# Optimization experiments

Measured on AMD Instinct MI355X. Metric: run time of the kernel, lower is better.

The kernel has to match this reference:

```python
import jax, jax.numpy as jnp
import numpy as np

D_MODEL = 1024
NUM_HEADS = 16
HEAD_DIM = D_MODEL // NUM_HEADS


def setup_inputs() -> dict:
    key = jax.random.key(0)
    ks = jax.random.split(key, 9)
    s = 1.0 / np.sqrt(D_MODEL)
    return {
        "x": jax.random.normal(ks[0], (4, 2048, D_MODEL), dtype=jnp.float32),
        "Wq": jax.random.uniform(ks[1], (D_MODEL, D_MODEL), minval=-s, maxval=s, dtype=jnp.float32),
        "bq": jax.random.uniform(ks[2], (D_MODEL,), minval=-s, maxval=s, dtype=jnp.float32),
        "Wk": jax.random.uniform(ks[3], (D_MODEL, D_MODEL), minval=-s, maxval=s, dtype=jnp.float32),
        "bk": jax.random.uniform(ks[4], (D_MODEL,), minval=-s, maxval=s, dtype=jnp.float32),
        "Wv": jax.random.uniform(ks[5], (D_MODEL, D_MODEL), minval=-s, maxval=s, dtype=jnp.float32),
        "bv": jax.random.uniform(ks[6], (D_MODEL,), minval=-s, maxval=s, dtype=jnp.float32),
        "Wo": jax.random.uniform(ks[7], (D_MODEL, D_MODEL), minval=-s, maxval=s, dtype=jnp.float32),
        "bo": jax.random.uniform(ks[8], (D_MODEL,), minval=-s, maxval=s, dtype=jnp.float32),
    }


def reference(x, Wq, bq, Wk, bk, Wv, bv, Wo, bo):
    B, T, C = x.shape
    H, Dh = NUM_HEADS, HEAD_DIM
    # projections (nn.Linear applies x @ W^T + b)
    q = (x @ Wq.T + bq).reshape(B, T, H, Dh).transpose(0, 2, 1, 3)  # [B,H,T,Dh]
    k = (x @ Wk.T + bk).reshape(B, T, H, Dh).transpose(0, 2, 1, 3)
    v = (x @ Wv.T + bv).reshape(B, T, H, Dh).transpose(0, 2, 1, 3)
    scale = 1.0 / np.sqrt(Dh).astype(np.float32)
    att = jnp.einsum("bhqd,bhkd->bhqk", q, k) * scale  # [B,H,T,T]
    causal = jnp.tril(jnp.ones((T, T), dtype=bool))
    att = jnp.where(causal[None, None], att, -jnp.inf)
    att = jax.nn.softmax(att, axis=-1)
    # dropout is identity in eval mode
    out = jnp.einsum("bhqk,bhkd->bhqd", att, v)  # [B,H,T,Dh]
    out = out.transpose(0, 2, 1, 3).reshape(B, T, C)
    return out @ Wo.T + bo
```

## Files before the change

kernel.cpp:

```cpp
#include <hip/hip_runtime.h>
#include <stdint.h>

typedef __attribute__((ext_vector_type(8))) short short8;
typedef __attribute__((ext_vector_type(4))) short short4v;
typedef __attribute__((ext_vector_type(4))) float floatx4;

#define QSCALE 0.1803368801111f

__device__ __forceinline__ unsigned short f2bf(float f) {
  unsigned int u = __float_as_uint(f);
  unsigned int r = (u + 0x7FFFu + ((u >> 16) & 1u)) >> 16;
  return (unsigned short)r;
}

__device__ __forceinline__ unsigned int cvt_pk_bf16(float lo, float hi) {
  unsigned int r;
  asm("v_cvt_pk_bf16_f32 %0, %1, %2" : "=v"(r) : "v"(lo), "v"(hi));
  return r;
}

__device__ __forceinline__ float max3f(float a, float b, float c) {
  float r;
  asm("v_max3_f32 %0, %1, %2, %3" : "=v"(r) : "v"(a), "v"(b), "v"(c));
  return r;
}

__device__ __forceinline__ float max16(const floatx4& a, const floatx4& b,
                                       const floatx4& c, const floatx4& d) {
  float m1 = max3f(a[0], a[1], a[2]);
  float m2 = max3f(a[3], b[0], b[1]);
  float m3 = max3f(b[2], b[3], c[0]);
  float m4 = max3f(c[1], c[2], c[3]);
  float m5 = max3f(d[0], d[1], d[2]);
  float r1 = max3f(m1, m2, m3);
  float r2 = max3f(m4, m5, d[3]);
  return fmaxf(r1, r2);
}

__device__ __forceinline__ void async_copy16(void* lds, const void* g) {
  __builtin_amdgcn_global_load_lds(
      (const __attribute__((address_space(1))) unsigned int*)g,
      (__attribute__((address_space(3))) unsigned int*)lds, 16, 0, 0);
}

__global__ __launch_bounds__(256) void f2ball_kernel(
    const float* __restrict__ x, unsigned short* __restrict__ xb,
    const float* __restrict__ w0, const float* __restrict__ w1,
    const float* __restrict__ w2, const float* __restrict__ w3,
    unsigned short* __restrict__ o0, unsigned short* __restrict__ o1,
    unsigned short* __restrict__ o2, unsigned short* __restrict__ o3) {
  const float* in;
  unsigned short* out;
  long i;
  if (blockIdx.x < 8192) {
    in = x;
    out = xb;
    i = (long)blockIdx.x * 256 + threadIdx.x;
  } else {
    int wb = blockIdx.x - 8192;
    int which = wb >> 10;
    in = (which == 0) ? w0 : (which == 1) ? w1 : (which == 2) ? w2 : w3;
    out = (which == 0) ? o0 : (which == 1) ? o1 : (which == 2) ? o2 : o3;
    i = (long)(wb & 1023) * 256 + threadIdx.x;
  }
  float4 v = ((const float4*)in)[i];
  short4v o;
  o[0] = (short)f2bf(v.x);
  o[1] = (short)f2bf(v.y);
  o[2] = (short)f2bf(v.z);
  o[3] = (short)f2bf(v.w);
  *(short4v*)(out + i * 4) = o;
}

__device__ __forceinline__ void gemm128_mainloop_db(
    const unsigned short* __restrict__ A, const unsigned short* __restrict__ Bt,
    int K, long brow, long bcol, unsigned short* As, unsigned short* Bs,
    floatx4 acc[4][4]) {
  const int tid = threadIdx.x;
  const int wave = tid >> 6;
  const int lane = tid & 63;
  const int wr = wave >> 1, wc = wave & 1;
  const int lr = lane & 15, lg = lane >> 4;

  const unsigned short* ga = A + (brow + (tid >> 2)) * (long)K + (tid & 3) * 8;
  const unsigned short* gb = Bt + (bcol + (tid >> 2)) * (long)K + (tid & 3) * 8;
  const int woff = wave * 512;
  const int a_off = (wr * 64 + lr) * 32 + lg * 8;
  const int b_off = (wc * 64 + lr) * 32 + lg * 8;

  async_copy16(As + woff, ga);
  async_copy16(As + woff + 2048, ga + (long)64 * K);
  async_copy16(Bs + woff, gb);
  async_copy16(Bs + woff + 2048, gb + (long)64 * K);
  ga += 32;
  gb += 32;
  __syncthreads();

  int buf = 0;
  for (int kt = 0; kt < K; kt += 32) {
    if (kt + 32 < K) {
      unsigned short* lA = As + (buf ^ 1) * 4096 + woff;
      unsigned short* lB = Bs + (buf ^ 1) * 4096 + woff;
      async_copy16(lA, ga);
      async_copy16(lA + 2048, ga + (long)64 * K);
      async_copy16(lB, gb);
      async_copy16(lB + 2048, gb + (long)64 * K);
      ga += 32;
      gb += 32;
    }
    const unsigned short* Ab = As + buf * 4096;
    const unsigned short* Bb = Bs + buf * 4096;
    short8 af[4], bf[4];
#pragma unroll
    for (int i = 0; i < 4; ++i) {
      af[i] = *(const short8*)(Ab + a_off + i * 512);
      bf[i] = *(const short8*)(Bb + b_off + i * 512);
    }
#pragma unroll
    for (int i = 0; i < 4; ++i)
#pragma unroll
      for (int j = 0; j < 4; ++j)
        acc[i][j] = __builtin_amdgcn_mfma_f32_16x16x32_bf16(af[i], bf[j], acc[i][j], 0, 0, 0);
    __syncthreads();
    buf ^= 1;
  }
}

__global__ __launch_bounds__(256, 4) void qkv_gemm(
    const unsigned short* __restrict__ xb, const unsigned short* __restrict__ wqkv,
    const float* __restrict__ bq, const float* __restrict__ bk,
    const float* __restrict__ bv, unsigned short* __restrict__ q_out,
    unsigned short* __restrict__ k_out, unsigned short* __restrict__ vt_out) {
  __shared__ __align__(16) unsigned short Sh[128 * 136];
  unsigned short* As = Sh;
  unsigned short* Bs = Sh + 8192;
  floatx4 zero = {0.f, 0.f, 0.f, 0.f};
  floatx4 acc[4][4];
#pragma unroll
  for (int i = 0; i < 4; ++i)
#pragma unroll
    for (int j = 0; j < 4; ++j) acc[i][j] = zero;

  long brow = (long)blockIdx.x * 128;
  long bcol = (long)blockIdx.y * 128;
  gemm128_mainloop_db(xb, wqkv, 1024, brow, bcol, As, Bs, acc);

  const int wave = threadIdx.x >> 6, lane = threadIdx.x & 63;
  const int wr = wave >> 1, wc = wave & 1, lr = lane & 15, lg = lane >> 4;
  const int kind = (int)(bcol >> 10);
  const float* bias = (kind == 0) ? bq : (kind == 1 ? bk : bv);

  if (kind == 2) {
#pragma unroll
    for (int i = 0; i < 4; ++i)
#pragma unroll
      for (int j = 0; j < 4; ++j) {
        int n_local = wc * 64 + j * 16 + lr;
        int m_base = wr * 64 + i * 16 + lg * 4;
        float bsc = bias[(int)((bcol + n_local) & 1023)];
        short4v pk;
#pragma unroll
        for (int r = 0; r < 4; ++r) pk[r] = (short)f2bf(acc[i][j][r] + bsc);
        *(short4v*)(Sh + n_local * 136 + m_base) = pk;
      }
    __syncthreads();
    const int b = (int)(brow >> 11);
    const int t0 = (int)(brow & 2047);
    const int f0 = (int)(bcol - 2048);
#pragma unroll
    for (int p = 0; p < 8; ++p) {
      int c = p * 256 + threadIdx.x;
      int d_loc = c >> 4, tc = c & 15;
      short8 v = *(const short8*)(Sh + d_loc * 136 + tc * 8);
      int h = (f0 >> 6) + (d_loc >> 6);
      int d = d_loc & 63;
      *(short8*)(vt_out + ((long)((b * 16 + h) * 64 + d)) * 2048 + t0 + tc * 8) = v;
    }
  } else {
#pragma unroll
    for (int i = 0; i < 4; ++i)
#pragma unroll
      for (int j = 0; j < 4; ++j)
#pragma unroll
        for (int r = 0; r < 4; ++r) {
          int m = (int)brow + wr * 64 + i * 16 + lg * 4 + r;
          int n = (int)bcol + wc * 64 + j * 16 + lr;
          int f = n & 1023;
          float v = acc[i][j][r] + bias[f];
          if (kind == 0) v *= QSCALE;
          unsigned short o = f2bf(v);
          int h = f >> 6, d = f & 63;
          int bb = m >> 11, t = m & 2047;
          long bh = (long)(bb * 16 + h);
          if (kind == 0)
            q_out[(bh * 2048 + t) * 64 + d] = o;
          else
            k_out[(bh * 2048 + t) * 64 + d] = o;
        }
  }
}

__global__ __launch_bounds__(256, 4) void out_gemm(
    const unsigned short* __restrict__ ob, const unsigned short* __restrict__ wo,
    const float* __restrict__ bo, float* __restrict__ out) {
  __shared__ unsigned short As[2 * 128 * 32];
  __shared__ unsigned short Bs[2 * 128 * 32];
  floatx4 zero = {0.f, 0.f, 0.f, 0.f};
  floatx4 acc[4][4];
#pragma unroll
  for (int i = 0; i < 4; ++i)
#pragma unroll
    for (int j = 0; j < 4; ++j) acc[i][j] = zero;

  long brow = (long)blockIdx.x * 128;
  long bcol = (long)blockIdx.y * 128;
  gemm128_mainloop_db(ob, wo, 1024, brow, bcol, As, Bs, acc);

  const int wave = threadIdx.x >> 6, lane = threadIdx.x & 63;
  const int wr = wave >> 1, wc = wave & 1, lr = lane & 15, lg = lane >> 4;
#pragma unroll
  for (int i = 0; i < 4; ++i)
#pragma unroll
    for (int j = 0; j < 4; ++j)
#pragma unroll
      for (int r = 0; r < 4; ++r) {
        int m = (int)brow + wr * 64 + i * 16 + lg * 4 + r;
        int n = (int)bcol + wc * 64 + j * 16 + lr;
        out[(long)m * 1024 + n] = acc[i][j][r] + bo[n];
      }
}

__device__ __forceinline__ void stage_kv(char* __restrict__ Kb, char* __restrict__ Vb,
                                         const char* __restrict__ Kp,
                                         const char* __restrict__ Vt, int kv0,
                                         int tid) {
  const int wave = tid >> 6;
#pragma unroll
  for (int j = 0; j < 2; ++j) {
    int d = j * 256 + tid;
    int row = d >> 3, cc = d & 7;
    int gc = cc ^ (row & 7);
    const char* gk = Kp + (size_t)kv0 * 128 + row * 128 + gc * 16;
    async_copy16(Kb + (j * 256 + wave * 64) * 16, gk);
    const char* gv = Vt + (size_t)row * 4096 + (size_t)kv0 * 2 + gc * 16;
    async_copy16(Vb + (j * 256 + wave * 64) * 16, gv);
  }
}

__device__ __forceinline__ void attn_step(
    const char* __restrict__ Kb, const char* __restrict__ Vb,
    char* __restrict__ PTw, const short8 (&qf)[2][2],
    int kv0, int q0, int lr, int lg, bool diag,
    float (&m_i)[2], floatx4 (&accL)[2], floatx4 (&accO)[2][4]) {
  floatx4 zero = {0.f, 0.f, 0.f, 0.f};
  const int x7 = lr & 7;
  floatx4 s[2][4];
  __builtin_amdgcn_s_setprio(1);
#pragma unroll
  for (int nt = 0; nt < 4; ++nt) {
    const char* kr = Kb + (nt * 16 + lr) * 128;
    short8 kf0 = *(const short8*)(kr + ((lg ^ x7) * 16));
    short8 kf1 = *(const short8*)(kr + (((4 + lg) ^ x7) * 16));
#pragma unroll
    for (int qa = 0; qa < 2; ++qa) {
      floatx4 a = zero;
      a = __builtin_amdgcn_mfma_f32_16x16x32_bf16(kf0, qf[qa][0], a, 0, 0, 0);
      a = __builtin_amdgcn_mfma_f32_16x16x32_bf16(kf1, qf[qa][1], a, 0, 0, 0);
      s[qa][nt] = a;
    }
  }
  __builtin_amdgcn_s_setprio(0);

  if (diag) {
#pragma unroll
    for (int qa = 0; qa < 2; ++qa) {
      const int q = q0 + qa * 16 + lr;
#pragma unroll
      for (int nt = 0; nt < 4; ++nt)
#pragma unroll
        for (int r = 0; r < 4; ++r) {
          int kvi = kv0 + nt * 16 + lg * 4 + r;
          if (kvi > q) s[qa][nt][r] = -1e30f;
        }
    }
  }

  float pmax[2];
#pragma unroll
  for (int qa = 0; qa < 2; ++qa)
    pmax[qa] = max16(s[qa][0], s[qa][1], s[qa][2], s[qa][3]);

  float g = fmaxf(pmax[0] - m_i[0], pmax[1] - m_i[1]);
  if (__any(g > 11.5f)) {
#pragma unroll
    for (int qa = 0; qa < 2; ++qa) {
      float mx = fmaxf(pmax[qa], __shfl_xor(pmax[qa], 16));
      mx = fmaxf(mx, __shfl_xor(mx, 32));
      float mnew = fmaxf(m_i[qa], mx);
      float scl = exp2f(m_i[qa] - mnew);
      m_i[qa] = mnew;
#pragma unroll
      for (int r = 0; r < 4; ++r) {
        float so = __shfl(scl, lg * 4 + r);
        accL[qa][r] *= so;
#pragma unroll
        for (int dt = 0; dt < 4; ++dt) accO[qa][dt][r] *= so;
      }
    }
  }

#pragma unroll
  for (int qa = 0; qa < 2; ++qa) {
    char* prow = PTw + (qa * 16 + lr) * 128;
#pragma unroll
    for (int nt = 0; nt < 4; ++nt) {
      float p0 = exp2f(s[qa][nt][0] - m_i[qa]);
      float p1 = exp2f(s[qa][nt][1] - m_i[qa]);
      float p2 = exp2f(s[qa][nt][2] - m_i[qa]);
      float p3 = exp2f(s[qa][nt][3] - m_i[qa]);
      uint2 wv;
      wv.x = cvt_pk_bf16(p0, p1);
      wv.y = cvt_pk_bf16(p2, p3);
      *(uint2*)(prow + (((2 * nt + (lg >> 1)) ^ x7) * 16) + ((2 * lg) & 3) * 4) = wv;
    }
  }

  short8 ones;
#pragma unroll
  for (int j = 0; j < 8; ++j) ones[j] = (short)0x3F80;

  __builtin_amdgcn_s_setprio(1);
#pragma unroll
  for (int kk = 0; kk < 2; ++kk) {
    short8 pf0 = *(const short8*)(PTw + lr * 128 + (((4 * kk + lg) ^ x7) * 16));
    short8 pf1 = *(const short8*)(PTw + (16 + lr) * 128 + (((4 * kk + lg) ^ x7) * 16));
#pragma unroll
    for (int dt = 0; dt < 4; ++dt) {
      short8 vf = *(const short8*)(Vb + (dt * 16 + lr) * 128 + (((4 * kk + lg) ^ x7) * 16));
      accO[0][dt] = __builtin_amdgcn_mfma_f32_16x16x32_bf16(pf0, vf, accO[0][dt], 0, 0, 0);
      accO[1][dt] = __builtin_amdgcn_mfma_f32_16x16x32_bf16(pf1, vf, accO[1][dt], 0, 0, 0);
    }
    accL[0] = __builtin_amdgcn_mfma_f32_16x16x32_bf16(pf0, ones, accL[0], 0, 0, 0);
    accL[1] = __builtin_amdgcn_mfma_f32_16x16x32_bf16(pf1, ones, accL[1], 0, 0, 0);
  }
  __builtin_amdgcn_s_setprio(0);
}

__global__ __launch_bounds__(256, 3) void attn_fwd(
    const unsigned short* __restrict__ qb, const unsigned short* __restrict__ kb,
    const unsigned short* __restrict__ vtb, unsigned short* __restrict__ ob) {
  __shared__ __align__(16) char Kbuf[2][8192];
  __shared__ __align__(16) char Vbuf[2][8192];
  __shared__ __align__(16) char PTbuf[4][4096];

  const int id = blockIdx.x;
  const int qt = 15 - (id >> 6);
  const int bh = id & 63;

  const int tid = threadIdx.x;
  const int wave = tid >> 6, lane = tid & 63;
  const int lr = lane & 15, lg = lane >> 4;
  const unsigned short* Q = qb + (long)bh * 2048 * 64;
  const char* Kp = (const char*)(kb + (long)bh * 2048 * 64);
  const char* Vt = (const char*)(vtb + (long)bh * 64 * 2048);
  const int b = bh >> 4, h = bh & 15;
  char* PTw = PTbuf[wave];

  floatx4 zero = {0.f, 0.f, 0.f, 0.f};

  const int q0 = qt * 128 + wave * 32;
  const int nkv = 2 * qt + 2;

  short8 qf[2][2];
#pragma unroll
  for (int qa = 0; qa < 2; ++qa)
#pragma unroll
    for (int kk = 0; kk < 2; ++kk)
      qf[qa][kk] = *(const short8*)(Q + (q0 + qa * 16 + lr) * 64 + kk * 32 + lg * 8);

  floatx4 accO[2][4];
  floatx4 accL[2];
#pragma unroll
  for (int qa = 0; qa < 2; ++qa) {
    accL[qa] = zero;
#pragma unroll
    for (int dt = 0; dt < 4; ++dt) accO[qa][dt] = zero;
  }
  float m_i[2] = {-1e30f, -1e30f};

  stage_kv(Kbuf[0], Vbuf[0], Kp, Vt, 0, tid);
  __syncthreads();
#pragma unroll 1
  for (int kv = 0; kv < nkv; ++kv) {
    if (kv + 1 < nkv)
      stage_kv(Kbuf[(kv + 1) & 1], Vbuf[(kv + 1) & 1], Kp, Vt, (kv + 1) * 64, tid);
    const int kv0 = kv * 64;
    if (kv0 < q0 + 32)
      attn_step(Kbuf[kv & 1], Vbuf[kv & 1], PTw, qf, kv0, q0, lr, lg,
                kv0 + 64 > q0, m_i, accL, accO);
    __syncthreads();
  }

#pragma unroll
  for (int qa = 0; qa < 2; ++qa) {
#pragma unroll
    for (int r = 0; r < 4; ++r) {
      float io = 1.f / accL[qa][r];
      int tq = q0 + qa * 16 + 4 * lg + r;
#pragma unroll
      for (int dt = 0; dt < 4; ++dt)
        ob[((long)b * 2048 + tq) * 1024 + h * 64 + dt * 16 + lr] =
            f2bf(accO[qa][dt][r] * io);
    }
  }
}

extern "C" void kernel_launch(void* const* d_in, const int* in_sizes, int n_in,
                              void* d_out, int out_size, void* d_ws, size_t ws_size,
                              hipStream_t stream) {
  const float* x = (const float*)d_in[0];
  const float* bq = (const float*)d_in[2];
  const float* bk = (const float*)d_in[4];
  const float* bv = (const float*)d_in[6];
  const float* bo = (const float*)d_in[8];
  float* out = (float*)d_out;

  char* ws = (char*)d_ws;
  unsigned short* xb = (unsigned short*)(ws);
  unsigned short* wqkv = (unsigned short*)(ws + (16l << 20));
  unsigned short* wob = (unsigned short*)(ws + (22l << 20));
  unsigned short* qb = (unsigned short*)(ws + (24l << 20));
  unsigned short* kb = (unsigned short*)(ws + (40l << 20));
  unsigned short* vtb = (unsigned short*)(ws + (56l << 20));
  unsigned short* ob = (unsigned short*)(ws + (72l << 20));

  f2ball_kernel<<<12288, 256, 0, stream>>>(
      x, xb, (const float*)d_in[1], (const float*)d_in[3], (const float*)d_in[5],
      (const float*)d_in[7], wqkv, wqkv + (1l << 20), wqkv + (2l << 20), wob);

  qkv_gemm<<<dim3(64, 24), 256, 0, stream>>>(xb, wqkv, bq, bk, bv, qb, kb, vtb);
  attn_fwd<<<1024, 256, 0, stream>>>(qb, kb, vtb, ob);
  out_gemm<<<dim3(64, 8), 256, 0, stream>>>(ob, wob, bo, out);
}
```

Baseline: 164.2 us.

## Fuse attention and output projection into one kernel with per-tile completion counters

Merges the attention kernel and the output GEMM into a single launch. The first 1024 blocks do attention and bump an atomic counter per (batch, query tile) once their output rows are written. The remaining 512 blocks spin-wait on the counter for their row tile, then run the output GEMM. This removes the kernel boundary and lets the output projection overlap with the tail of attention. In exchange it adds a memset launch, spin-wait blocks that hold CU slots, and a deadlock risk if waiting blocks get scheduled before the attention blocks they depend on. The counters sit at the start of the workspace, which is also where xb lives, but qkv_gemm has already consumed xb before the memset.

```diff
diff --git a/kernel.cpp b/kernel.cpp
--- a/kernel.cpp
+++ b/kernel.cpp
@@ -200,36 +200,6 @@
   }
 }
 
-__global__ __launch_bounds__(256, 4) void out_gemm(
-    const unsigned short* __restrict__ ob, const unsigned short* __restrict__ wo,
-    const float* __restrict__ bo, float* __restrict__ out) {
-  __shared__ unsigned short As[2 * 128 * 32];
-  __shared__ unsigned short Bs[2 * 128 * 32];
-  floatx4 zero = {0.f, 0.f, 0.f, 0.f};
-  floatx4 acc[4][4];
-#pragma unroll
-  for (int i = 0; i < 4; ++i)
-#pragma unroll
-    for (int j = 0; j < 4; ++j) acc[i][j] = zero;
-
-  long brow = (long)blockIdx.x * 128;
-  long bcol = (long)blockIdx.y * 128;
-  gemm128_mainloop_db(ob, wo, 1024, brow, bcol, As, Bs, acc);
-
-  const int wave = threadIdx.x >> 6, lane = threadIdx.x & 63;
-  const int wr = wave >> 1, wc = wave & 1, lr = lane & 15, lg = lane >> 4;
-#pragma unroll
-  for (int i = 0; i < 4; ++i)
-#pragma unroll
-    for (int j = 0; j < 4; ++j)
-#pragma unroll
-      for (int r = 0; r < 4; ++r) {
-        int m = (int)brow + wr * 64 + i * 16 + lg * 4 + r;
-        int n = (int)bcol + wc * 64 + j * 16 + lr;
-        out[(long)m * 1024 + n] = acc[i][j][r] + bo[n];
-      }
-}
-
 __device__ __forceinline__ void stage_kv(char* __restrict__ Kb, char* __restrict__ Vb,
                                          const char* __restrict__ Kp,
                                          const char* __restrict__ Vt, int kv0,
@@ -346,72 +316,117 @@
   __builtin_amdgcn_s_setprio(0);
 }
 
-__global__ __launch_bounds__(256, 3) void attn_fwd(
+__global__ __launch_bounds__(256, 3) void attn_out_fused(
     const unsigned short* __restrict__ qb, const unsigned short* __restrict__ kb,
-    const unsigned short* __restrict__ vtb, unsigned short* __restrict__ ob) {
-  __shared__ __align__(16) char Kbuf[2][8192];
-  __shared__ __align__(16) char Vbuf[2][8192];
-  __shared__ __align__(16) char PTbuf[4][4096];
-
-  const int id = blockIdx.x;
-  const int qt = 15 - (id >> 6);
-  const int bh = id & 63;
-
+    const unsigned short* __restrict__ vtb, unsigned short* __restrict__ ob,
+    const unsigned short* __restrict__ wo, const float* __restrict__ bo,
+    float* __restrict__ out, unsigned int* __restrict__ cnt) {
+  __shared__ __align__(16) char Lds[49152];
   const int tid = threadIdx.x;
-  const int wave = tid >> 6, lane = tid & 63;
-  const int lr = lane & 15, lg = lane >> 4;
-  const unsigned short* Q = qb + (long)bh * 2048 * 64;
-  const char* Kp = (const char*)(kb + (long)bh * 2048 * 64);
-  const char* Vt = (const char*)(vtb + (long)bh * 64 * 2048);
-  const int b = bh >> 4, h = bh & 15;
-  char* PTw = PTbuf[wave];
-
   floatx4 zero = {0.f, 0.f, 0.f, 0.f};
 
-  const int q0 = qt * 128 + wave * 32;
-  const int nkv = 2 * qt + 2;
-
-  short8 qf[2][2];
-#pragma unroll
-  for (int qa = 0; qa < 2; ++qa)
-#pragma unroll
-    for (int kk = 0; kk < 2; ++kk)
-      qf[qa][kk] = *(const short8*)(Q + (q0 + qa * 16 + lr) * 64 + kk * 32 + lg * 8);
-
-  floatx4 accO[2][4];
-  floatx4 accL[2];
-#pragma unroll
-  for (int qa = 0; qa < 2; ++qa) {
-    accL[qa] = zero;
-#pragma unroll
-    for (int dt = 0; dt < 4; ++dt) accO[qa][dt] = zero;
-  }
-  float m_i[2] = {-1e30f, -1e30f};
-
-  stage_kv(Kbuf[0], Vbuf[0], Kp, Vt, 0, tid);
-  __syncthreads();
+  if (blockIdx.x < 1024) {
+    char* Kbuf = Lds;
+    char* Vbuf = Lds + 16384;
+    char* PTb = Lds + 32768;
+
+    const int id = blockIdx.x;
+    const int qt = 15 - (id >> 6);
+    const int bh = id & 63;
+
+    const int wave = tid >> 6, lane = tid & 63;
+    const int lr = lane & 15, lg = lane >> 4;
+    const unsigned short* Q = qb + (long)bh * 2048 * 64;
+    const char* Kp = (const char*)(kb + (long)bh * 2048 * 64);
+    const char* Vt = (const char*)(vtb + (long)bh * 64 * 2048);
+    const int b = bh >> 4, h = bh & 15;
+    char* PTw = PTb + wave * 4096;
+
+    const int q0 = qt * 128 + wave * 32;
+    const int nkv = 2 * qt + 2;
+
+    short8 qf[2][2];
+#pragma unroll
+    for (int qa = 0; qa < 2; ++qa)
+#pragma unroll
+      for (int kk = 0; kk < 2; ++kk)
+        qf[qa][kk] = *(const short8*)(Q + (q0 + qa * 16 + lr) * 64 + kk * 32 + lg * 8);
+
+    floatx4 accO[2][4];
+    floatx4 accL[2];
+#pragma unroll
+    for (int qa = 0; qa < 2; ++qa) {
+      accL[qa] = zero;
+#pragma unroll
+      for (int dt = 0; dt < 4; ++dt) accO[qa][dt] = zero;
+    }
+    float m_i[2] = {-1e30f, -1e30f};
+
+    stage_kv(Kbuf, Vbuf, Kp, Vt, 0, tid);
+    __syncthreads();
 #pragma unroll 1
-  for (int kv = 0; kv < nkv; ++kv) {
-    if (kv + 1 < nkv)
-      stage_kv(Kbuf[(kv + 1) & 1], Vbuf[(kv + 1) & 1], Kp, Vt, (kv + 1) * 64, tid);
-    const int kv0 = kv * 64;
-    if (kv0 < q0 + 32)
-      attn_step(Kbuf[kv & 1], Vbuf[kv & 1], PTw, qf, kv0, q0, lr, lg,
-                kv0 + 64 > q0, m_i, accL, accO);
+    for (int kv = 0; kv < nkv; ++kv) {
+      if (kv + 1 < nkv)
+        stage_kv(Kbuf + ((kv + 1) & 1) * 8192, Vbuf + ((kv + 1) & 1) * 8192, Kp, Vt,
+                 (kv + 1) * 64, tid);
+      const int kv0 = kv * 64;
+      if (kv0 < q0 + 32)
+        attn_step(Kbuf + (kv & 1) * 8192, Vbuf + (kv & 1) * 8192, PTw, qf, kv0, q0,
+                  lr, lg, kv0 + 64 > q0, m_i, accL, accO);
+      __syncthreads();
+    }
+
+#pragma unroll
+    for (int qa = 0; qa < 2; ++qa) {
+#pragma unroll
+      for (int r = 0; r < 4; ++r) {
+        float io = 1.f / accL[qa][r];
+        int tq = q0 + qa * 16 + 4 * lg + r;
+#pragma unroll
+        for (int dt = 0; dt < 4; ++dt)
+          ob[((long)b * 2048 + tq) * 1024 + h * 64 + dt * 16 + lr] =
+              f2bf(accO[qa][dt][r] * io);
+      }
+    }
     __syncthreads();
-  }
-
-#pragma unroll
-  for (int qa = 0; qa < 2; ++qa) {
-#pragma unroll
-    for (int r = 0; r < 4; ++r) {
-      float io = 1.f / accL[qa][r];
-      int tq = q0 + qa * 16 + 4 * lg + r;
-#pragma unroll
-      for (int dt = 0; dt < 4; ++dt)
-        ob[((long)b * 2048 + tq) * 1024 + h * 64 + dt * 16 + lr] =
-            f2bf(accO[qa][dt][r] * io);
-    }
+    if (tid == 0) {
+      __threadfence();
+      atomicAdd(&cnt[b * 16 + qt], 1u);
+    }
+  } else {
+    const int oid = blockIdx.x - 1024;
+    long brow = (long)(oid >> 3) * 128;
+    long bcol = (long)(oid & 7) * 128;
+
+    if (tid == 0) {
+      while (atomicAdd(&cnt[(int)(brow >> 7)], 0u) < 16u)
+        __builtin_amdgcn_s_sleep(8);
+    }
+    __syncthreads();
+    __threadfence();
+
+    unsigned short* As = (unsigned short*)Lds;
+    unsigned short* Bs = (unsigned short*)(Lds + 16384);
+    floatx4 acc[4][4];
+#pragma unroll
+    for (int i = 0; i < 4; ++i)
+#pragma unroll
+      for (int j = 0; j < 4; ++j) acc[i][j] = zero;
+
+    gemm128_mainloop_db(ob, wo, 1024, brow, bcol, As, Bs, acc);
+
+    const int wave = tid >> 6, lane = tid & 63;
+    const int wr = wave >> 1, wc = wave & 1, lr = lane & 15, lg = lane >> 4;
+#pragma unroll
+    for (int i = 0; i < 4; ++i)
+#pragma unroll
+      for (int j = 0; j < 4; ++j)
+#pragma unroll
+        for (int r = 0; r < 4; ++r) {
+          int m = (int)brow + wr * 64 + i * 16 + lg * 4 + r;
+          int n = (int)bcol + wc * 64 + j * 16 + lr;
+          out[(long)m * 1024 + n] = acc[i][j][r] + bo[n];
+        }
   }
 }
 
@@ -433,12 +448,15 @@
   unsigned short* kb = (unsigned short*)(ws + (40l << 20));
   unsigned short* vtb = (unsigned short*)(ws + (56l << 20));
   unsigned short* ob = (unsigned short*)(ws + (72l << 20));
+  unsigned int* cnt = (unsigned int*)ws;
 
   f2ball_kernel<<<12288, 256, 0, stream>>>(
       x, xb, (const float*)d_in[1], (const float*)d_in[3], (const float*)d_in[5],
       (const float*)d_in[7], wqkv, wqkv + (1l << 20), wqkv + (2l << 20), wob);
 
   qkv_gemm<<<dim3(64, 24), 256, 0, stream>>>(xb, wqkv, bq, bk, bv, qb, kb, vtb);
-  attn_fwd<<<1024, 256, 0, stream>>>(qb, kb, vtb, ob);
-  out_gemm<<<dim3(64, 8), 256, 0, stream>>>(ob, wob, bo, out);
-}
+
+  hipMemsetAsync(cnt, 0, 64 * sizeof(unsigned int), stream);
+
+  attn_out_fused<<<1536, 256, 0, stream>>>(qb, kb, vtb, ob, wob, bo, out, cnt);
+}
```

After: 273.6 us. 1.67x slower.

## Widen QKV GEMM tile to 128x256 with per-wave 64x128 outputs

Applied to the files above, without the earlier changes.

Replaces the 128x128 QKV projection GEMM with a 128x256-tile kernel where each wave accumulates a 4x8 grid of MFMA tiles, doubling B-operand reuse per A fragment and halving the grid to 768 blocks. The kernel has its own inlined double-buffered async-copy main loop with s_setprio around the MFMA burst. The V-transpose epilogue is split into two halves so it fits the shared-memory staging buffer. Costs are higher register pressure (launch bounds drop to 2 blocks per SM), fewer blocks to fill the GPU, and an extra synchronization pass in the V epilogue.

```diff
diff --git a/kernel.cpp b/kernel.cpp
--- a/kernel.cpp
+++ b/kernel.cpp
@@ -126,65 +126,121 @@
   }
 }
 
-__global__ __launch_bounds__(256, 4) void qkv_gemm(
+__global__ __launch_bounds__(256, 2) void qkv_gemm256(
     const unsigned short* __restrict__ xb, const unsigned short* __restrict__ wqkv,
     const float* __restrict__ bq, const float* __restrict__ bk,
     const float* __restrict__ bv, unsigned short* __restrict__ q_out,
     unsigned short* __restrict__ k_out, unsigned short* __restrict__ vt_out) {
-  __shared__ __align__(16) unsigned short Sh[128 * 136];
+  __shared__ __align__(16) unsigned short Sh[24576];
   unsigned short* As = Sh;
   unsigned short* Bs = Sh + 8192;
+
+  const int tid = threadIdx.x;
+  const int wave = tid >> 6, lane = tid & 63;
+  const int wr = wave >> 1, wc = wave & 1;
+  const int lr = lane & 15, lg = lane >> 4;
+
+  const long brow = (long)blockIdx.x * 128;
+  const long bcol = (long)blockIdx.y * 256;
+
   floatx4 zero = {0.f, 0.f, 0.f, 0.f};
-  floatx4 acc[4][4];
+  floatx4 acc[4][8];
 #pragma unroll
   for (int i = 0; i < 4; ++i)
 #pragma unroll
-    for (int j = 0; j < 4; ++j) acc[i][j] = zero;
-
-  long brow = (long)blockIdx.x * 128;
-  long bcol = (long)blockIdx.y * 128;
-  gemm128_mainloop_db(xb, wqkv, 1024, brow, bcol, As, Bs, acc);
-
-  const int wave = threadIdx.x >> 6, lane = threadIdx.x & 63;
-  const int wr = wave >> 1, wc = wave & 1, lr = lane & 15, lg = lane >> 4;
+    for (int j = 0; j < 8; ++j) acc[i][j] = zero;
+
+  const int K = 1024;
+  const unsigned short* ga = xb + (brow + (tid >> 2)) * (long)K + (tid & 3) * 8;
+  const unsigned short* gb = wqkv + (bcol + (tid >> 2)) * (long)K + (tid & 3) * 8;
+  const int woff = wave * 512;
+  const int a_off = (wr * 64 + lr) * 32 + lg * 8;
+  const int b_off = (wc * 128 + lr) * 32 + lg * 8;
+
+  async_copy16(As + woff, ga);
+  async_copy16(As + woff + 2048, ga + (long)64 * K);
+#pragma unroll
+  for (int jj = 0; jj < 4; ++jj)
+    async_copy16(Bs + woff + jj * 2048, gb + (long)jj * 64 * K);
+  ga += 32;
+  gb += 32;
+  __syncthreads();
+
+  int buf = 0;
+  for (int kt = 0; kt < K; kt += 32) {
+    if (kt + 32 < K) {
+      unsigned short* lA = As + (buf ^ 1) * 4096 + woff;
+      unsigned short* lB = Bs + (buf ^ 1) * 8192 + woff;
+      async_copy16(lA, ga);
+      async_copy16(lA + 2048, ga + (long)64 * K);
+#pragma unroll
+      for (int jj = 0; jj < 4; ++jj)
+        async_copy16(lB + jj * 2048, gb + (long)jj * 64 * K);
+      ga += 32;
+      gb += 32;
+    }
+    const unsigned short* Ab = As + buf * 4096;
+    const unsigned short* Bb = Bs + buf * 8192;
+    short8 av[4], bvf[8];
+#pragma unroll
+    for (int i = 0; i < 4; ++i) av[i] = *(const short8*)(Ab + a_off + i * 512);
+#pragma unroll
+    for (int j = 0; j < 8; ++j) bvf[j] = *(const short8*)(Bb + b_off + j * 512);
+    __builtin_amdgcn_s_setprio(1);
+#pragma unroll
+    for (int i = 0; i < 4; ++i)
+#pragma unroll
+      for (int j = 0; j < 8; ++j)
+        acc[i][j] = __builtin_amdgcn_mfma_f32_16x16x32_bf16(av[i], bvf[j], acc[i][j], 0, 0, 0);
+    __builtin_amdgcn_s_setprio(0);
+    __syncthreads();
+    buf ^= 1;
+  }
+
   const int kind = (int)(bcol >> 10);
   const float* bias = (kind == 0) ? bq : (kind == 1 ? bk : bv);
 
   if (kind == 2) {
+#pragma unroll 1
+    for (int half = 0; half < 2; ++half) {
+      if (wc == half) {
+#pragma unroll
+        for (int i = 0; i < 4; ++i)
+#pragma unroll
+          for (int j = 0; j < 8; ++j) {
+            int n_local = j * 16 + lr;
+            int m_base = wr * 64 + i * 16 + lg * 4;
+            float bsc = bias[(int)((bcol + half * 128 + n_local) & 1023)];
+            short4v pk;
+#pragma unroll
+            for (int r = 0; r < 4; ++r) pk[r] = (short)f2bf(acc[i][j][r] + bsc);
+            *(short4v*)(Sh + n_local * 136 + m_base) = pk;
+          }
+      }
+      __syncthreads();
+      const int b = (int)(brow >> 11);
+      const int t0 = (int)(brow & 2047);
+      const int f0h = (int)(bcol - 2048) + half * 128;
+#pragma unroll
+      for (int p = 0; p < 8; ++p) {
+        int c = p * 256 + tid;
+        int d_loc = c >> 4, tc = c & 15;
+        short8 v = *(const short8*)(Sh + d_loc * 136 + tc * 8);
+        int h = (f0h >> 6) + (d_loc >> 6);
+        int d = d_loc & 63;
+        *(short8*)(vt_out + ((long)((b * 16 + h) * 64 + d)) * 2048 + t0 + tc * 8) = v;
+      }
+      __syncthreads();
+    }
+  } else {
 #pragma unroll
     for (int i = 0; i < 4; ++i)
 #pragma unroll
-      for (int j = 0; j < 4; ++j) {
-        int n_local = wc * 64 + j * 16 + lr;
-        int m_base = wr * 64 + i * 16 + lg * 4;
-        float bsc = bias[(int)((bcol + n_local) & 1023)];
-        short4v pk;
-#pragma unroll
-        for (int r = 0; r < 4; ++r) pk[r] = (short)f2bf(acc[i][j][r] + bsc);
-        *(short4v*)(Sh + n_local * 136 + m_base) = pk;
-      }
-    __syncthreads();
-    const int b = (int)(brow >> 11);
-    const int t0 = (int)(brow & 2047);
-    const int f0 = (int)(bcol - 2048);
-#pragma unroll
-    for (int p = 0; p < 8; ++p) {
-      int c = p * 256 + threadIdx.x;
-      int d_loc = c >> 4, tc = c & 15;
-      short8 v = *(const short8*)(Sh + d_loc * 136 + tc * 8);
-      int h = (f0 >> 6) + (d_loc >> 6);
-      int d = d_loc & 63;
-      *(short8*)(vt_out + ((long)((b * 16 + h) * 64 + d)) * 2048 + t0 + tc * 8) = v;
-    }
-  } else {
-#pragma unroll
-    for (int i = 0; i < 4; ++i)
-#pragma unroll
-      for (int j = 0; j < 4; ++j)
+      for (int j = 0; j < 8; ++j)
 #pragma unroll
         for (int r = 0; r < 4; ++r) {
           int m = (int)brow + wr * 64 + i * 16 + lg * 4 + r;
-          int n = (int)bcol + wc * 64 + j * 16 + lr;
+          int n = (int)bcol + wc * 128 + j * 16 + lr;
           int f = n & 1023;
           float v = acc[i][j][r] + bias[f];
           if (kind == 0) v *= QSCALE;
@@ -438,7 +494,7 @@
       x, xb, (const float*)d_in[1], (const float*)d_in[3], (const float*)d_in[5],
       (const float*)d_in[7], wqkv, wqkv + (1l << 20), wqkv + (2l << 20), wob);
 
-  qkv_gemm<<<dim3(64, 24), 256, 0, stream>>>(xb, wqkv, bq, bk, bv, qb, kb, vtb);
+  qkv_gemm256<<<dim3(64, 12), 256, 0, stream>>>(xb, wqkv, bq, bk, bv, qb, kb, vtb);
   attn_fwd<<<1024, 256, 0, stream>>>(qb, kb, vtb, ob);
   out_gemm<<<dim3(64, 8), 256, 0, stream>>>(ob, wob, bo, out);
 }
```

After: 164.4 us. About the same (+0.1%).
